# Kernel tuning notes

Hardware: AMD Instinct MI355X
Metric: run time of the kernel (lower is better)

The kernel has to match this reference:

```python
import jax, jax.numpy as jnp
import numpy as np

B, T, U = 8, 200, 50
EPROJS = 512
DUNITS = 512
EMB = 512
JOINT = 512
ODIM = 1000
BLANK = 0


def setup_inputs() -> dict:
    key = jax.random.key(0)
    ks = jax.random.split(key, 16)
    s = lambda k, shape: (jax.random.normal(k, shape, jnp.float32) * 0.05)
    inp = {
        "hs_pad": jax.random.normal(ks[0], (B, T, EPROJS), jnp.float32),
        "ys_in_pad": jax.random.randint(ks[1], (B, U), 0, ODIM),
        "emb": s(ks[2], (ODIM, EMB)),
        "W_ih_0": s(ks[3], (4 * DUNITS, EMB)),
        "W_hh_0": s(ks[4], (4 * DUNITS, DUNITS)),
        "b_ih_0": s(ks[5], (4 * DUNITS,)),
        "b_hh_0": s(ks[6], (4 * DUNITS,)),
        "W_ih_1": s(ks[7], (4 * DUNITS, DUNITS)),
        "W_hh_1": s(ks[8], (4 * DUNITS, DUNITS)),
        "b_ih_1": s(ks[9], (4 * DUNITS,)),
        "b_hh_1": s(ks[10], (4 * DUNITS,)),
        "W_enc": s(ks[11], (JOINT, EPROJS)),
        "b_enc": s(ks[12], (JOINT,)),
        "W_dec": s(ks[13], (JOINT, DUNITS)),
        "W_out": s(ks[14], (ODIM, JOINT)),
        "b_out": s(ks[15], (ODIM,)),
    }
    return inp


def _lstm_cell(x, h, c, W_ih, W_hh, b_ih, b_hh):
    # torch.nn.LSTMCell, gate order i, f, g, o
    gates = x @ W_ih.T + b_ih + h @ W_hh.T + b_hh
    i, f, g, o = jnp.split(gates, 4, axis=-1)
    c_new = jax.nn.sigmoid(f) * c + jax.nn.sigmoid(i) * jnp.tanh(g)
    h_new = jax.nn.sigmoid(o) * jnp.tanh(c_new)
    return h_new, c_new


def reference(hs_pad, ys_in_pad, emb, W_ih_0, W_hh_0, b_ih_0, b_hh_0,
              W_ih_1, W_hh_1, b_ih_1, b_hh_1, W_enc, b_enc, W_dec,
              W_out, b_out):
    # embedding with padding_idx=blank -> blank row is zero
    emb_tbl = emb.at[BLANK].set(0.0)
    eys = emb_tbl[ys_in_pad]            # (B, U, EMB)

    def step(carry, ey):
        h0, c0, h1, c1 = carry
        h0, c0 = _lstm_cell(ey, h0, c0, W_ih_0, W_hh_0, b_ih_0, b_hh_0)
        h1, c1 = _lstm_cell(h0, h1, c1, W_ih_1, W_hh_1, b_ih_1, b_hh_1)
        return (h0, c0, h1, c1), h1

    z0 = jnp.zeros((hs_pad.shape[0], DUNITS), hs_pad.dtype)
    _, h_dec = jax.lax.scan(step, (z0, z0, z0, z0),
                            jnp.swapaxes(eys, 0, 1))   # (U, B, D)
    h_dec = jnp.swapaxes(h_dec, 0, 1)                  # (B, U, D)

    # joint: project first, then broadcast-add (avoids (B,T,U,Henc) expand)
    z_enc = hs_pad @ W_enc.T + b_enc                   # (B, T, J)
    z_dec = h_dec @ W_dec.T                            # (B, U, J), no bias
    z = jnp.tanh(z_enc[:, :, None, :] + z_dec[:, None, :, :])  # (B,T,U,J)
    return z @ W_out.T + b_out                         # (B, T, U, ODIM)
```

## Files before the change

kernel.cpp:

```cpp
#include <hip/hip_runtime.h>
#include <cstdint>
#include <cstddef>

#define Tsz 200
#define Usz 50
#define Kd  512
#define G4h 2048
#define OD  1000

typedef __attribute__((ext_vector_type(8))) short short8;
typedef __attribute__((ext_vector_type(4))) short s16x4;
typedef __attribute__((ext_vector_type(4))) float f32x4;
typedef __attribute__((ext_vector_type(16))) float f32x16;

__device__ __forceinline__ unsigned short f2bf(float x) {
  union { float f; unsigned u; } v; v.f = x;
  unsigned r = v.u + 0x7FFFu + ((v.u >> 16) & 1u);
  return (unsigned short)(r >> 16);
}
__device__ __forceinline__ float bf2f(unsigned short h) {
  union { unsigned u; float f; } v; v.u = ((unsigned)h) << 16; return v.f;
}
__device__ __forceinline__ void splits(float w, short& hi, short& lo) {
  unsigned short h = f2bf(w);
  hi = (short)h;
  lo = (short)f2bf(w - bf2f(h));
}
__device__ __forceinline__ void split8(float4 f0, float4 f1, short8& hi, short8& lo) {
  float v[8] = {f0.x, f0.y, f0.z, f0.w, f1.x, f1.y, f1.z, f1.w};
  #pragma unroll
  for (int i = 0; i < 8; ++i) { short a, b2; splits(v[i], a, b2); hi[i] = a; lo[i] = b2; }
}
__device__ __forceinline__ float ftanh(float x) {
  float ax = fabsf(x);
  float t = __expf(-2.0f * ax);
  float r = (1.0f - t) / (1.0f + t);
  return copysignf(r, x);
}
__device__ __forceinline__ float sigf(float x) {
  return 1.0f / (1.0f + __expf(-x));
}
__device__ __forceinline__ void astore(unsigned* p, unsigned v) {
  __hip_atomic_store(p, v, __ATOMIC_RELAXED, __HIP_MEMORY_SCOPE_AGENT);
}
__device__ __forceinline__ void gload16(const void* g, void* l) {
  __builtin_amdgcn_global_load_lds(
      (const __attribute__((address_space(1))) void*)g,
      (__attribute__((address_space(3))) void*)l, 16, 0, 0);
}
__device__ __forceinline__ void aload4x4(const unsigned* p0, const unsigned* p1,
                                         const unsigned* p2, const unsigned* p3,
                                         uint4& r0, uint4& r1, uint4& r2, uint4& r3) {
  asm volatile(
      "global_load_dwordx4 %0, %4, off sc0 sc1\n\t"
      "global_load_dwordx4 %1, %5, off sc0 sc1\n\t"
      "global_load_dwordx4 %2, %6, off sc0 sc1\n\t"
      "global_load_dwordx4 %3, %7, off sc0 sc1\n\t"
      "s_waitcnt vmcnt(0)"
      : "=&v"(r0), "=&v"(r1), "=&v"(r2), "=&v"(r3)
      : "v"(p0), "v"(p1), "v"(p2), "v"(p3)
      : "memory");
}
__device__ __forceinline__ void aload8x4(const unsigned* p0, const unsigned* p1,
                                         const unsigned* p2, const unsigned* p3,
                                         const unsigned* q0, const unsigned* q1,
                                         const unsigned* q2, const unsigned* q3,
                                         uint4& r0, uint4& r1, uint4& r2, uint4& r3,
                                         uint4& s0, uint4& s1, uint4& s2, uint4& s3) {
  asm volatile(
      "global_load_dwordx4 %0, %8, off sc0 sc1\n\t"
      "global_load_dwordx4 %1, %9, off sc0 sc1\n\t"
      "global_load_dwordx4 %2, %10, off sc0 sc1\n\t"
      "global_load_dwordx4 %3, %11, off sc0 sc1\n\t"
      "global_load_dwordx4 %4, %12, off sc0 sc1\n\t"
      "global_load_dwordx4 %5, %13, off sc0 sc1\n\t"
      "global_load_dwordx4 %6, %14, off sc0 sc1\n\t"
      "global_load_dwordx4 %7, %15, off sc0 sc1\n\t"
      "s_waitcnt vmcnt(0)"
      : "=&v"(r0), "=&v"(r1), "=&v"(r2), "=&v"(r3),
        "=&v"(s0), "=&v"(s1), "=&v"(s2), "=&v"(s3)
      : "v"(p0), "v"(p1), "v"(p2), "v"(p3),
        "v"(q0), "v"(q1), "v"(q2), "v"(q3)
      : "memory");
}
__device__ __forceinline__ unsigned tagbad4(uint4 v, unsigned tg) {
  return ((v.x ^ tg) | (v.y ^ tg) | (v.z ^ tg) | (v.w ^ tg)) & 0xFFu;
}

__global__ __launch_bounds__(256) void k_prep(
    const int* __restrict__ ys, const float* __restrict__ emb,
    const float* __restrict__ Wih0, const float* __restrict__ bih0,
    const float* __restrict__ bhh0,
    unsigned* __restrict__ h0s, unsigned* __restrict__ h1s,
    float* __restrict__ xgr) {
  __shared__ float Al[16 * 516];
  __shared__ int idxs[16];
  const int bid = blockIdx.x;
  const int tid = threadIdx.x;

  if (bid < 16) {
    int i = bid * 256 + tid;
    if (i < 4096) { h0s[i] = 0u; h1s[i] = 0u; }
    return;
  }
  int q = bid - 16;
  int m0 = (q % 25) * 16;
  int n0 = (q / 25) * 64;
  if (tid < 16) {
    int m = m0 + tid;
    int u = m >> 3, b = m & 7;
    idxs[tid] = ys[b * Usz + u];
  }
  __syncthreads();
  for (int i = tid; i < 16 * 512; i += 256) {
    int r = i >> 9, k = i & 511;
    int idx = idxs[r];
    Al[r * 516 + k] = (idx == 0) ? 0.0f : emb[(size_t)idx * Kd + k];
  }
  __syncthreads();
  int nl = tid & 63;
  int mg = (tid >> 6) * 4;
  int n = n0 + nl;
  const float* Wr = Wih0 + (size_t)n * Kd;
  float acc[4] = {0.f, 0.f, 0.f, 0.f};
  #pragma unroll 4
  for (int k = 0; k < 512; k += 4) {
    float4 w = *(const float4*)(Wr + k);
    #pragma unroll
    for (int j = 0; j < 4; ++j) {
      const float* ar = &Al[(mg + j) * 516 + k];
      acc[j] += ar[0] * w.x + ar[1] * w.y + ar[2] * w.z + ar[3] * w.w;
    }
  }
  float bias = bih0[n] + bhh0[n];
  int g = n >> 9, jc = n & 511;
  #pragma unroll
  for (int j = 0; j < 4; ++j) {
    int m = m0 + mg + j;
    int u = m >> 3, b = m & 7;
    xgr[(((size_t)u * 32 + (jc >> 4)) * 4 + g) * 128 + (jc & 15) * 8 + b] =
        acc[j] + bias;
  }
}

__global__ __launch_bounds__(256) void k_gemm(const float* __restrict__ A,
                                              const float* __restrict__ W,
                                              float* __restrict__ C, int N) {
  __shared__ float Al[16 * 516];
  int m0 = blockIdx.x * 16;
  int n0 = blockIdx.y * 64;
  for (int i = threadIdx.x; i < 16 * 512; i += 256) {
    int r = i >> 9, k = i & 511;
    Al[r * 516 + k] = A[(size_t)(m0 + r) * Kd + k];
  }
  __syncthreads();
  int nl = threadIdx.x & 63;
  int mg = (threadIdx.x >> 6) * 4;
  int n = n0 + nl;
  const float* Wr = W + (size_t)n * Kd;
  float acc[4] = {0.f, 0.f, 0.f, 0.f};
  #pragma unroll 4
  for (int k = 0; k < 512; k += 4) {
    float4 w = *(const float4*)(Wr + k);
    #pragma unroll
    for (int j = 0; j < 4; ++j) {
      const float* ar = &Al[(mg + j) * 516 + k];
      acc[j] += ar[0] * w.x + ar[1] * w.y + ar[2] * w.z + ar[3] * w.w;
    }
  }
  #pragma unroll
  for (int j = 0; j < 4; ++j)
    C[(size_t)(m0 + mg + j) * N + n] = acc[j];
}

__global__ __launch_bounds__(256, 1) void k_lstm_zenc(
    const float* __restrict__ Whh0, const float* __restrict__ Wih1,
    const float* __restrict__ Whh1, const float* __restrict__ bih1,
    const float* __restrict__ bhh1, const float* __restrict__ xgr,
    unsigned* __restrict__ h0s, unsigned* __restrict__ h1s,
    float* __restrict__ hdec,
    const float* __restrict__ Wout, unsigned short* __restrict__ Wb,
    const float* __restrict__ hs, const float* __restrict__ Wenc,
    const float* __restrict__ benc, float* __restrict__ zenc) {
  __shared__ __align__(16) unsigned short sd[34816];
  unsigned short* H0H = sd;
  unsigned short* H0L = sd + 8192;
  unsigned short* H1H = sd + 16384;
  unsigned short* H1L = sd + 24576;
  float* gsm = (float*)(sd + 32768);

  const int tid = threadIdx.x;
  const int lane = tid & 63;
  const int wv = tid >> 6;
  const int bid = blockIdx.x;

  if (bid >= 352) {
    float* Al = (float*)sd;
    int q = bid - 352;
    int m0 = (q % 100) * 16;
    int n0 = (q / 100) * 64;
    for (int i = tid; i < 16 * 512; i += 256) {
      int r = i >> 9, k = i & 511;
      Al[r * 516 + k] = hs[(size_t)(m0 + r) * Kd + k];
    }
    __syncthreads();
    int nl = tid & 63;
    int mg = (tid >> 6) * 4;
    int n = n0 + nl;
    const float* Wr = Wenc + (size_t)n * Kd;
    float acc[4] = {0.f, 0.f, 0.f, 0.f};
    #pragma unroll 4
    for (int k = 0; k < 512; k += 4) {
      float4 w = *(const float4*)(Wr + k);
      #pragma unroll
      for (int j = 0; j < 4; ++j) {
        const float* ar = &Al[(mg + j) * 516 + k];
        acc[j] += ar[0] * w.x + ar[1] * w.y + ar[2] * w.z + ar[3] * w.w;
      }
    }
    float bias = benc[n];
    #pragma unroll
    for (int j = 0; j < 4; ++j)
      zenc[(size_t)(m0 + mg + j) * 512 + n] = acc[j] + bias;
    return;
  }
  if (bid >= 96) {
    int idx = (bid - 96) * 256 + tid;
    int n = idx >> 6, chunk = idx & 63;
    short8 v;
    if (n < OD) {
      const float* src = Wout + (size_t)n * Kd + chunk * 8;
      #pragma unroll
      for (int j = 0; j < 8; ++j) v[j] = (short)f2bf(src[j]);
    } else {
      #pragma unroll
      for (int j = 0; j < 8; ++j) v[j] = 0;
    }
    int tile = n >> 5, srow = n & 31;
    size_t off = (size_t)tile * 32768 + srow * 1024 +
                 ((chunk * 16) ^ (srow << 4));
    *(short8*)((char*)Wb + off) = v;
    return;
  }

  const int kq = lane >> 4;
  const int cl = lane & 15;
  const int gg = (tid & 127) >> 1;
  const int sub = (tid & 1) << 3;
  const int swz = (gg & 7) << 4;
  const int gbase = gg << 8;
  const int tb = tid >> 7;

  if (bid < 32) {
    const int j0 = bid * 16;
    short8 whi[16], wlo[16];
    {
      const float* wr = Whh0 + ((size_t)(wv * 512 + j0 + cl)) * Kd;
      #pragma unroll
      for (int kt = 0; kt < 16; ++kt) {
        const float* p4 = wr + kt * 32 + kq * 8;
        split8(*(const float4*)p4, *(const float4*)(p4 + 4), whi[kt], wlo[kt]);
      }
    }
    float creg = 0.0f;
    const int ejl = tid & 15, eb = (tid >> 4) & 7;
    for (int p = 0; p < 50; ++p) {
      const float* xp = xgr + (((size_t)p * 32 + bid) * 4) * 128 + ejl * 8 + eb;
      float x0 = xp[0], x1 = xp[128], x2 = xp[256], x3 = xp[384];
      {
        const unsigned* bp = h0s + (size_t)p * 4096 + (tid << 2);
        uint4 v0, v1, v2, v3;
        aload4x4(bp, bp + 1024, bp + 2048, bp + 3072, v0, v1, v2, v3);
        const unsigned tg = (unsigned)p;
        for (int guard = 0; guard < (1 << 18); ++guard) {
          unsigned bad = tagbad4(v0, tg) | tagbad4(v1, tg) |
                         tagbad4(v2, tg) | tagbad4(v3, tg);
          if (!bad) break;
          __builtin_amdgcn_s_sleep(1);
          aload4x4(bp, bp + 1024, bp + 2048, bp + 3072, v0, v1, v2, v3);
        }
        unsigned uu[4][4] = {{v0.x, v0.y, v0.z, v0.w}, {v1.x, v1.y, v1.z, v1.w},
                             {v2.x, v2.y, v2.z, v2.w}, {v3.x, v3.y, v3.z, v3.w}};
        #pragma unroll
        for (int j = 0; j < 4; ++j) {
          s16x4 hv, lv;
          #pragma unroll
          for (int e = 0; e < 4; ++e) {
            short hh, ll; splits(__uint_as_float(uu[j][e]), hh, ll);
            hv[e] = hh; lv[e] = ll;
          }
          int b = j * 2 + tb;
          int off = gbase + (((b << 4) + sub) ^ swz);
          *(s16x4*)((char*)H0H + off) = hv;
          *(s16x4*)((char*)H0L + off) = lv;
        }
      }
      __syncthreads();
      f32x4 accA = {0.f, 0.f, 0.f, 0.f};
      f32x4 accB = {0.f, 0.f, 0.f, 0.f};
      f32x4 accC = {0.f, 0.f, 0.f, 0.f};
      #pragma unroll
      for (int kt = 0; kt < 16; ++kt) {
        int g = kt * 4 + kq;
        int off = (g << 8) + ((cl << 4) ^ ((g & 7) << 4));
        short8 bh = *(const short8*)((const char*)H0H + off);
        short8 bl = *(const short8*)((const char*)H0L + off);
        accA = __builtin_amdgcn_mfma_f32_16x16x32_bf16(whi[kt], bh, accA, 0, 0, 0);
        accB = __builtin_amdgcn_mfma_f32_16x16x32_bf16(wlo[kt], bh, accB, 0, 0, 0);
        accC = __builtin_amdgcn_mfma_f32_16x16x32_bf16(whi[kt], bl, accC, 0, 0, 0);
      }
      f32x4 acc = (accA + accB) + accC;
      *(f32x4*)&gsm[(wv * 16 + cl) * 16 + kq * 4] = acc;
      __syncthreads();
      if (tid < 128) {
        float g0 = gsm[(0 * 16 + eb) * 16 + ejl];
        float g1 = gsm[(1 * 16 + eb) * 16 + ejl];
        float g2 = gsm[(2 * 16 + eb) * 16 + ejl];
        float g3 = gsm[(3 * 16 + eb) * 16 + ejl];
        float gi = g0 + x0;
        float gf = g1 + x1;
        float gg2 = g2 + x2;
        float go = g3 + x3;
        float cn = sigf(gf) * creg + sigf(gi) * ftanh(gg2);
        float hn = sigf(go) * ftanh(cn);
        creg = cn;
        unsigned hv = (__float_as_uint(hn) & ~0xFFu) | (unsigned)(p + 1);
        astore(h0s + (size_t)(p + 1) * 4096 + eb * 512 + j0 + ejl, hv);
      }
      __syncthreads();
    }
  } else {
    const int j0 = (bid - 32) * 8;
    const int mt = wv & 1, kh = wv >> 1;
    short8 wihh[8], wihl[8], whhh[8], whhl[8];
    {
      const int g = mt * 2 + (cl >> 3), jl = cl & 7;
      const float* wr0 = Wih1 + ((size_t)(g * 512 + j0 + jl)) * Kd;
      const float* wr1 = Whh1 + ((size_t)(g * 512 + j0 + jl)) * Kd;
      #pragma unroll
      for (int k2 = 0; k2 < 8; ++k2) {
        int kt = kh * 8 + k2;
        const float* p0 = wr0 + kt * 32 + kq * 8;
        const float* p1 = wr1 + kt * 32 + kq * 8;
        split8(*(const float4*)p0, *(const float4*)(p0 + 4), wihh[k2], wihl[k2]);
        split8(*(const float4*)p1, *(const float4*)(p1 + 4), whhh[k2], whhl[k2]);
      }
    }
    float creg = 0.0f;
    const int ejl = tid & 7, eb = (tid >> 3) & 7;
    float bs0 = bih1[0 * 512 + j0 + ejl] + bhh1[0 * 512 + j0 + ejl];
    float bs1 = bih1[1 * 512 + j0 + ejl] + bhh1[1 * 512 + j0 + ejl];
    float bs2 = bih1[2 * 512 + j0 + ejl] + bhh1[2 * 512 + j0 + ejl];
    float bs3 = bih1[3 * 512 + j0 + ejl] + bhh1[3 * 512 + j0 + ejl];
    for (int p = 1; p <= 50; ++p) {
      {
        const unsigned* bp0 = h0s + (size_t)p * 4096 + (tid << 2);
        const unsigned* bp1 = h1s + (size_t)(p - 1) * 4096 + (tid << 2);
        uint4 v0, v1, v2, v3, w0, w1, w2, w3;
        aload8x4(bp0, bp0 + 1024, bp0 + 2048, bp0 + 3072,
                 bp1, bp1 + 1024, bp1 + 2048, bp1 + 3072,
                 v0, v1, v2, v3, w0, w1, w2, w3);
        const unsigned tg0 = (unsigned)p, tg1 = (unsigned)(p - 1);
        for (int guard = 0; guard < (1 << 18); ++guard) {
          unsigned bad = tagbad4(v0, tg0) | tagbad4(v1, tg0) |
                         tagbad4(v2, tg0) | tagbad4(v3, tg0) |
                         tagbad4(w0, tg1) | tagbad4(w1, tg1) |
                         tagbad4(w2, tg1) | tagbad4(w3, tg1);
          if (!bad) break;
          __builtin_amdgcn_s_sleep(1);
          aload8x4(bp0, bp0 + 1024, bp0 + 2048, bp0 + 3072,
                   bp1, bp1 + 1024, bp1 + 2048, bp1 + 3072,
                   v0, v1, v2, v3, w0, w1, w2, w3);
        }
        unsigned uu[4][4] = {{v0.x, v0.y, v0.z, v0.w}, {v1.x, v1.y, v1.z, v1.w},
                             {v2.x, v2.y, v2.z, v2.w}, {v3.x, v3.y, v3.z, v3.w}};
        unsigned tt[4][4] = {{w0.x, w0.y, w0.z, w0.w}, {w1.x, w1.y, w1.z, w1.w},
                             {w2.x, w2.y, w2.z, w2.w}, {w3.x, w3.y, w3.z, w3.w}};
        #pragma unroll
        for (int j = 0; j < 4; ++j) {
          s16x4 hv, lv, hw, lw;
          #pragma unroll
          for (int e = 0; e < 4; ++e) {
            short hh, ll;
            splits(__uint_as_float(uu[j][e]), hh, ll); hv[e] = hh; lv[e] = ll;
            splits(__uint_as_float(tt[j][e]), hh, ll); hw[e] = hh; lw[e] = ll;
          }
          int b = j * 2 + tb;
          int off = gbase + (((b << 4) + sub) ^ swz);
          *(s16x4*)((char*)H0H + off) = hv;
          *(s16x4*)((char*)H0L + off) = lv;
          *(s16x4*)((char*)H1H + off) = hw;
          *(s16x4*)((char*)H1L + off) = lw;
        }
      }
      __syncthreads();
      f32x4 q0 = {0.f,0.f,0.f,0.f}, q1 = {0.f,0.f,0.f,0.f}, q2 = {0.f,0.f,0.f,0.f};
      f32x4 q3 = {0.f,0.f,0.f,0.f}, q4 = {0.f,0.f,0.f,0.f}, q5 = {0.f,0.f,0.f,0.f};
      #pragma unroll
      for (int k2 = 0; k2 < 8; ++k2) {
        int kt = kh * 8 + k2;
        int g = kt * 4 + kq;
        int off = (g << 8) + ((cl << 4) ^ ((g & 7) << 4));
        short8 b0h = *(const short8*)((const char*)H0H + off);
        short8 b0l = *(const short8*)((const char*)H0L + off);
        short8 b1h = *(const short8*)((const char*)H1H + off);
        short8 b1l = *(const short8*)((const char*)H1L + off);
        q0 = __builtin_amdgcn_mfma_f32_16x16x32_bf16(wihh[k2], b0h, q0, 0, 0, 0);
        q1 = __builtin_amdgcn_mfma_f32_16x16x32_bf16(wihl[k2], b0h, q1, 0, 0, 0);
        q2 = __builtin_amdgcn_mfma_f32_16x16x32_bf16(wihh[k2], b0l, q2, 0, 0, 0);
        q3 = __builtin_amdgcn_mfma_f32_16x16x32_bf16(whhh[k2], b1h, q3, 0, 0, 0);
        q4 = __builtin_amdgcn_mfma_f32_16x16x32_bf16(whhl[k2], b1h, q4, 0, 0, 0);
        q5 = __builtin_amdgcn_mfma_f32_16x16x32_bf16(whhh[k2], b1l, q5, 0, 0, 0);
      }
      f32x4 acc = ((q0 + q1) + (q2 + q3)) + (q4 + q5);
      *(f32x4*)&gsm[(wv * 16 + cl) * 16 + kq * 4] = acc;
      __syncthreads();
      if (tid < 64) {
        float gv[4];
        #pragma unroll
        for (int g = 0; g < 4; ++g) {
          int mtg = g >> 1, r = (g & 1) * 8 + ejl;
          gv[g] = gsm[(mtg * 16 + eb) * 16 + r] + gsm[((2 + mtg) * 16 + eb) * 16 + r];
        }
        float gi = gv[0] + bs0, gf = gv[1] + bs1, gg2 = gv[2] + bs2, go = gv[3] + bs3;
        float cn = sigf(gf) * creg + sigf(gi) * ftanh(gg2);
        float hn = sigf(go) * ftanh(cn);
        creg = cn;
        int jg = j0 + ejl;
        unsigned hv = (__float_as_uint(hn) & ~0xFFu) | (unsigned)p;
        astore(h1s + (size_t)p * 4096 + eb * 512 + jg, hv);
        hdec[((size_t)eb * Usz + (p - 1)) * Kd + jg] = __uint_as_float(hv);
      }
      __syncthreads();
    }
  }
}

__global__ __launch_bounds__(256, 1) void k_joint(
    const float* __restrict__ zenc, const float* __restrict__ zdec,
    const unsigned short* __restrict__ Wb, const float* __restrict__ bout,
    float* __restrict__ out) {
  __shared__ __align__(16) unsigned short Blds[2 * 16384];
  __shared__ float blds[1024];
  const int lane = threadIdx.x & 63;
  const int wv = threadIdx.x >> 6;
  const int r32 = lane & 31;
  const int kh = lane >> 5;
  const int rbase = blockIdx.x * 128 + wv * 32;

  for (int i = threadIdx.x; i < 1024; i += 256)
    blds[i] = (i < OD) ? bout[i] : 0.0f;

  short8 a[32];
  {
    int row = rbase + r32;
    int u = row % Usz;
    int bt = row / Usz;
    const float* ze = zenc + (size_t)bt * Kd;
    const float* zd = zdec + (size_t)((bt / Tsz) * Usz + u) * Kd;
    #pragma unroll
    for (int kt = 0; kt < 32; ++kt) {
      int k0 = kt * 16 + kh * 8;
      float4 e0 = *(const float4*)(ze + k0);
      float4 e1 = *(const float4*)(ze + k0 + 4);
      float4 d0 = *(const float4*)(zd + k0);
      float4 d1 = *(const float4*)(zd + k0 + 4);
      short8 tt;
      tt[0] = (short)f2bf(ftanh(e0.x + d0.x));
      tt[1] = (short)f2bf(ftanh(e0.y + d0.y));
      tt[2] = (short)f2bf(ftanh(e0.z + d0.z));
      tt[3] = (short)f2bf(ftanh(e0.w + d0.w));
      tt[4] = (short)f2bf(ftanh(e1.x + d1.x));
      tt[5] = (short)f2bf(ftanh(e1.y + d1.y));
      tt[6] = (short)f2bf(ftanh(e1.z + d1.z));
      tt[7] = (short)f2bf(ftanh(e1.w + d1.w));
      a[kt] = tt;
    }
  }

  #pragma unroll
  for (int i = 0; i < 8; ++i) {
    int o = (i * 4 + wv) * 1024;
    gload16((const char*)Wb + o + lane * 16, (char*)Blds + o);
  }
  asm volatile("s_waitcnt vmcnt(0)" ::: "memory");
  __builtin_amdgcn_s_barrier();
  __builtin_amdgcn_sched_barrier(0);

  int cur = 0;
  for (int it = 0; it < 32; ++it) {
    if (it < 31) {
      const char* g = (const char*)Wb + (size_t)(it + 1) * 32768;
      char* l = (char*)Blds + (cur ^ 1) * 32768;
      #pragma unroll
      for (int i = 0; i < 8; ++i) {
        int o = (i * 4 + wv) * 1024;
        gload16(g + o + lane * 16, l + o);
      }
      __builtin_amdgcn_sched_barrier(0);
    }
    const char* bufc = (const char*)Blds + cur * 32768;
    int n0 = it * 32;
    f32x16 accE = {0.f,0.f,0.f,0.f,0.f,0.f,0.f,0.f,0.f,0.f,0.f,0.f,0.f,0.f,0.f,0.f};
    f32x16 accO = {0.f,0.f,0.f,0.f,0.f,0.f,0.f,0.f,0.f,0.f,0.f,0.f,0.f,0.f,0.f,0.f};
    #pragma unroll
    for (int kt = 0; kt < 32; kt += 2) {
      int c0 = kt * 2 + kh;
      int c1 = c0 + 2;
      int o0 = r32 * 1024 + ((c0 * 16) ^ (r32 << 4));
      int o1 = r32 * 1024 + ((c1 * 16) ^ (r32 << 4));
      short8 b0 = *(const short8*)(bufc + o0);
      short8 b1 = *(const short8*)(bufc + o1);
      accE = __builtin_amdgcn_mfma_f32_32x32x16_bf16(a[kt], b0, accE, 0, 0, 0);
      accO = __builtin_amdgcn_mfma_f32_32x32x16_bf16(a[kt + 1], b1, accO, 0, 0, 0);
    }
    f32x16 acc = accE + accO;
    int n = n0 + r32;
    float bo = blds[n];
    if (n < OD) {
      size_t base = (size_t)(rbase + kh * 4) * OD + n;
      #pragma unroll
      for (int reg = 0; reg < 16; ++reg) {
        int r = (reg & 3) + 8 * (reg >> 2);
        out[base + (size_t)r * OD] = acc[reg] + bo;
      }
    }
    if (it < 31) {
      __builtin_amdgcn_sched_barrier(0);
      asm volatile("s_waitcnt vmcnt(16)" ::: "memory");
      __builtin_amdgcn_s_barrier();
      __builtin_amdgcn_sched_barrier(0);
    }
    cur ^= 1;
  }
}

extern "C" void kernel_launch(void* const* d_in, const int* in_sizes, int n_in,
                              void* d_out, int out_size, void* d_ws, size_t ws_size,
                              hipStream_t stream) {
  const float* hs   = (const float*)d_in[0];
  const int*   ys   = (const int*)d_in[1];
  const float* emb  = (const float*)d_in[2];
  const float* Wih0 = (const float*)d_in[3];
  const float* Whh0 = (const float*)d_in[4];
  const float* bih0 = (const float*)d_in[5];
  const float* bhh0 = (const float*)d_in[6];
  const float* Wih1 = (const float*)d_in[7];
  const float* Whh1 = (const float*)d_in[8];
  const float* bih1 = (const float*)d_in[9];
  const float* bhh1 = (const float*)d_in[10];
  const float* Wenc = (const float*)d_in[11];
  const float* benc = (const float*)d_in[12];
  const float* Wdec = (const float*)d_in[13];
  const float* Wout = (const float*)d_in[14];
  const float* bout = (const float*)d_in[15];
  float* out = (float*)d_out;

  float* ws   = (float*)d_ws;
  float* xgr  = ws + 204800;
  float* zenc = ws + 1024000;
  float* zdec = ws + 1843200;
  float* hdec = ws + 2048000;
  unsigned short* Wb = (unsigned short*)(ws + 2252800);
  unsigned* h0s = (unsigned*)(ws + 2514944);
  unsigned* h1s = (unsigned*)(ws + 2723840);

  k_prep<<<816, 256, 0, stream>>>(ys, emb, Wih0, bih0, bhh0, h0s, h1s, xgr);
  k_lstm_zenc<<<1152, 256, 0, stream>>>(Whh0, Wih1, Whh1, bih1, bhh1, xgr,
                                        h0s, h1s, hdec, Wout, Wb,
                                        hs, Wenc, benc, zenc);
  k_gemm<<<dim3(25, 8), 256, 0, stream>>>(hdec, Wdec, zdec, 512);
  k_joint<<<625, 256, 0, stream>>>(zenc, zdec, Wb, bout, out);
}
```

Before: 437.9 us.

## Fuse decoder projection into LSTM kernel via per-step tagged-flag consumer blocks

Removes the separate k_gemm launch for z_dec. Fifty extra blocks are appended to the LSTM kernel. Each one spin-waits, with backoff sleep, until the tagged h1 state for its step is published, then computes that step's W_dec projection. This overlaps the z_dec GEMM with the sequential recurrence and drops the hdec buffer and one kernel launch. It risks spinning blocks taking CU slots and relies on those blocks being co-resident. The k_joint launch bounds are also changed to a waves_per_eu attribute.

```diff
diff --git a/kernel.cpp b/kernel.cpp
--- a/kernel.cpp
+++ b/kernel.cpp
@@ -86,6 +86,9 @@
 __device__ __forceinline__ unsigned tagbad4(uint4 v, unsigned tg) {
   return ((v.x ^ tg) | (v.y ^ tg) | (v.z ^ tg) | (v.w ^ tg)) & 0xFFu;
 }
+__device__ __forceinline__ void bsleep(int slp) {
+  for (int s = 0; s < slp; ++s) __builtin_amdgcn_s_sleep(16);
+}
 
 __global__ __launch_bounds__(256) void k_prep(
     const int* __restrict__ ys, const float* __restrict__ emb,
@@ -143,45 +146,15 @@
   }
 }
 
-__global__ __launch_bounds__(256) void k_gemm(const float* __restrict__ A,
-                                              const float* __restrict__ W,
-                                              float* __restrict__ C, int N) {
-  __shared__ float Al[16 * 516];
-  int m0 = blockIdx.x * 16;
-  int n0 = blockIdx.y * 64;
-  for (int i = threadIdx.x; i < 16 * 512; i += 256) {
-    int r = i >> 9, k = i & 511;
-    Al[r * 516 + k] = A[(size_t)(m0 + r) * Kd + k];
-  }
-  __syncthreads();
-  int nl = threadIdx.x & 63;
-  int mg = (threadIdx.x >> 6) * 4;
-  int n = n0 + nl;
-  const float* Wr = W + (size_t)n * Kd;
-  float acc[4] = {0.f, 0.f, 0.f, 0.f};
-  #pragma unroll 4
-  for (int k = 0; k < 512; k += 4) {
-    float4 w = *(const float4*)(Wr + k);
-    #pragma unroll
-    for (int j = 0; j < 4; ++j) {
-      const float* ar = &Al[(mg + j) * 516 + k];
-      acc[j] += ar[0] * w.x + ar[1] * w.y + ar[2] * w.z + ar[3] * w.w;
-    }
-  }
-  #pragma unroll
-  for (int j = 0; j < 4; ++j)
-    C[(size_t)(m0 + mg + j) * N + n] = acc[j];
-}
-
 __global__ __launch_bounds__(256, 1) void k_lstm_zenc(
     const float* __restrict__ Whh0, const float* __restrict__ Wih1,
     const float* __restrict__ Whh1, const float* __restrict__ bih1,
     const float* __restrict__ bhh1, const float* __restrict__ xgr,
     unsigned* __restrict__ h0s, unsigned* __restrict__ h1s,
-    float* __restrict__ hdec,
     const float* __restrict__ Wout, unsigned short* __restrict__ Wb,
     const float* __restrict__ hs, const float* __restrict__ Wenc,
-    const float* __restrict__ benc, float* __restrict__ zenc) {
+    const float* __restrict__ benc, float* __restrict__ zenc,
+    const float* __restrict__ Wdec, float* __restrict__ zdec) {
   __shared__ __align__(16) unsigned short sd[34816];
   unsigned short* H0H = sd;
   unsigned short* H0L = sd + 8192;
@@ -194,6 +167,54 @@
   const int wv = tid >> 6;
   const int bid = blockIdx.x;
 
+  if (bid >= 1152) {
+    float* hl = (float*)sd;
+    const int u = bid - 1152;
+    const int p = u + 1;
+    {
+      const unsigned* bp = h1s + (size_t)p * 4096 + tid * 16;
+      uint4 v0, v1, v2, v3;
+      aload4x4(bp, bp + 4, bp + 8, bp + 12, v0, v1, v2, v3);
+      const unsigned tg = (unsigned)p & 0xFFu;
+      int slp = 1;
+      for (int guard = 0; guard < (1 << 14); ++guard) {
+        unsigned bad = tagbad4(v0, tg) | tagbad4(v1, tg) |
+                       tagbad4(v2, tg) | tagbad4(v3, tg);
+        if (!bad) break;
+        bsleep(slp);
+        if (slp < 8) slp <<= 1;
+        aload4x4(bp, bp + 4, bp + 8, bp + 12, v0, v1, v2, v3);
+      }
+      *(uint4*)&hl[tid * 16] = v0;
+      *(uint4*)&hl[tid * 16 + 4] = v1;
+      *(uint4*)&hl[tid * 16 + 8] = v2;
+      *(uint4*)&hl[tid * 16 + 12] = v3;
+    }
+    __syncthreads();
+    const int n2 = tid * 2;
+    const float* w0p = Wdec + (size_t)n2 * Kd;
+    const float* w1p = w0p + Kd;
+    float acc0[8] = {0, 0, 0, 0, 0, 0, 0, 0};
+    float acc1[8] = {0, 0, 0, 0, 0, 0, 0, 0};
+    #pragma unroll 4
+    for (int kc = 0; kc < 128; ++kc) {
+      float4 w0 = *(const float4*)(w0p + kc * 4);
+      float4 w1 = *(const float4*)(w1p + kc * 4);
+      #pragma unroll
+      for (int b = 0; b < 8; ++b) {
+        float4 h4 = *(const float4*)&hl[b * 512 + kc * 4];
+        acc0[b] += w0.x * h4.x + w0.y * h4.y + w0.z * h4.z + w0.w * h4.w;
+        acc1[b] += w1.x * h4.x + w1.y * h4.y + w1.z * h4.z + w1.w * h4.w;
+      }
+    }
+    #pragma unroll
+    for (int b = 0; b < 8; ++b) {
+      size_t base = ((size_t)(b * Usz + u) << 9);
+      zdec[base + n2] = acc0[b];
+      zdec[base + n2 + 1] = acc1[b];
+    }
+    return;
+  }
   if (bid >= 352) {
     float* Al = (float*)sd;
     int q = bid - 352;
@@ -429,14 +450,15 @@
         int jg = j0 + ejl;
         unsigned hv = (__float_as_uint(hn) & ~0xFFu) | (unsigned)p;
         astore(h1s + (size_t)p * 4096 + eb * 512 + jg, hv);
-        hdec[((size_t)eb * Usz + (p - 1)) * Kd + jg] = __uint_as_float(hv);
       }
       __syncthreads();
     }
   }
 }
 
-__global__ __launch_bounds__(256, 1) void k_joint(
+__global__ __launch_bounds__(256)
+__attribute__((amdgpu_waves_per_eu(1, 1)))
+void k_joint(
     const float* __restrict__ zenc, const float* __restrict__ zdec,
     const unsigned short* __restrict__ Wb, const float* __restrict__ bout,
     float* __restrict__ out) {
@@ -560,15 +582,13 @@
   float* xgr  = ws + 204800;
   float* zenc = ws + 1024000;
   float* zdec = ws + 1843200;
-  float* hdec = ws + 2048000;
   unsigned short* Wb = (unsigned short*)(ws + 2252800);
   unsigned* h0s = (unsigned*)(ws + 2514944);
   unsigned* h1s = (unsigned*)(ws + 2723840);
 
   k_prep<<<816, 256, 0, stream>>>(ys, emb, Wih0, bih0, bhh0, h0s, h1s, xgr);
-  k_lstm_zenc<<<1152, 256, 0, stream>>>(Whh0, Wih1, Whh1, bih1, bhh1, xgr,
-                                        h0s, h1s, hdec, Wout, Wb,
-                                        hs, Wenc, benc, zenc);
-  k_gemm<<<dim3(25, 8), 256, 0, stream>>>(hdec, Wdec, zdec, 512);
+  k_lstm_zenc<<<1202, 256, 0, stream>>>(Whh0, Wih1, Whh1, bih1, bhh1, xgr,
+                                        h0s, h1s, Wout, Wb,
+                                        hs, Wenc, benc, zenc, Wdec, zdec);
   k_joint<<<625, 256, 0, stream>>>(zenc, zdec, Wb, bout, out);
 }
```

New measurement: 415.6 us. 1.05x faster.
